# Kernel tuning notes

Measured on AMD Instinct MI355X. Metric: run time of the kernel, lower is better.

The kernel has to match this reference:

```python
import jax, jax.numpy as jnp
import numpy as np

S, T, C, L_GNN, L_TF, H = 8, 16, 128, 3, 2, 4
B = 512
FF = 4 * C
EPS = 1e-5


def setup_inputs() -> dict:
    key = jax.random.key(0)
    ks = jax.random.split(key, 24)
    w = lambda k, shape: jax.random.normal(k, shape, jnp.float32) * 0.05
    inp = {}
    inp["xx"] = jax.random.randint(ks[0], (B, T, S, S, S), 0, 3, dtype=jnp.int32)
    inp["ss"] = jax.random.uniform(ks[1], (B, 1), jnp.float32)
    # DynamicGNNv2 params
    inp["Win"] = w(ks[2], (C, 5)); inp["b_in"] = w(ks[3], (C,))
    inp["Wl"] = w(ks[4], (L_GNN, C, C)); inp["bl"] = w(ks[5], (L_GNN, C))   # SAGEConv lin_l (neighbors)
    inp["Wr"] = w(ks[6], (L_GNN, C, C))                                      # SAGEConv lin_r (root, no bias)
    inp["ln_g"] = jnp.ones((C,), jnp.float32); inp["ln_b"] = jnp.zeros((C,), jnp.float32)  # shared LayerNorm
    # TransformerEncoder params (norm_first, relu, dropout=0 at eval)
    inp["Wqkv"] = w(ks[7], (L_TF, 3 * C, C)); inp["bqkv"] = w(ks[8], (L_TF, 3 * C))
    inp["Wo"] = w(ks[9], (L_TF, C, C)); inp["bo"] = w(ks[10], (L_TF, C))
    inp["ln1_g"] = jnp.ones((L_TF, C), jnp.float32); inp["ln1_b"] = jnp.zeros((L_TF, C), jnp.float32)
    inp["ln2_g"] = jnp.ones((L_TF, C), jnp.float32); inp["ln2_b"] = jnp.zeros((L_TF, C), jnp.float32)
    inp["W1"] = w(ks[11], (L_TF, FF, C)); inp["b1"] = w(ks[12], (L_TF, FF))
    inp["W2"] = w(ks[13], (L_TF, C, FF)); inp["b2"] = w(ks[14], (L_TF, C))
    inp["Wact"] = w(ks[15], (C, S ** 3)); inp["bact"] = w(ks[16], (C,))
    inp["Wsc"] = w(ks[17], (C, 1)); inp["bsc"] = w(ks[18], (C,))
    return inp


def layernorm(x, g, b):
    mu = x.mean(-1, keepdims=True)
    var = ((x - mu) ** 2).mean(-1, keepdims=True)
    return (x - mu) * jax.lax.rsqrt(var + EPS) * g + b


def reference(xx, ss, Win, b_in, Wl, bl, Wr, ln_g, ln_b, Wqkv, bqkv, Wo, bo,
              ln1_g, ln1_b, ln2_g, ln2_b, W1, b1, W2, b2, Wact, bact, Wsc, bsc):
    Bc = xx.shape[0]
    S3 = S ** 3
    frame0 = xx[:, 0].reshape(Bc, S3).astype(jnp.float32)            # (B,S^3)
    m = (frame0 != 0).astype(jnp.float32)                            # active-node mask
    grid = jnp.arange(S3)
    i, j, k = grid // (S * S), (grid // S) % S, grid % S
    coord = jnp.stack([i, j, k], -1).astype(jnp.float32) / (S - 1)   # (S^3,3)
    feat = jnp.concatenate([
        jnp.broadcast_to(coord, (Bc, S3, 3)),
        (frame0 / 2.0)[..., None],
        jnp.broadcast_to((ss / S)[:, None, :], (Bc, S3, 1)),
    ], -1)                                                            # (B,S^3,5)
    x = feat @ Win.T + b_in                                           # lin_in
    mm = m[..., None]
    n = m.sum(-1, keepdims=True)[..., None]                           # nodes per graph (B,1,1)
    for l in range(L_GNN):
        # complete graph (no self loops): mean over neighbors = (sum_active - self)/(N-1)
        s = (x * mm).sum(1, keepdims=True)                            # (B,1,C)
        neigh = jnp.where(n > 1, (s - x) / jnp.maximum(n - 1.0, 1.0), 0.0)
        h = neigh @ Wl[l].T + bl[l] + x @ Wr[l].T                     # SAGEConv
        x = layernorm(jax.nn.relu(h), ln_g, ln_b)
    full = x * mm                                                     # scatter-fill into dense (B,S^3,C)
    # pooling matmul: mean over each i/j/k slice -> (B,3S,C)
    poolW = jnp.concatenate([
        (i[None, :] == jnp.arange(S)[:, None]).astype(jnp.float32),
        (j[None, :] == jnp.arange(S)[:, None]).astype(jnp.float32),
        (k[None, :] == jnp.arange(S)[:, None]).astype(jnp.float32),
    ], 0)                                                             # (3S,S^3)
    gnn_emb = jnp.einsum('ps,bsc->bpc', poolW, full) / poolW.sum(1)[None, :, None]
    # transformer over past actions
    a = xx[:, 1:].reshape(Bc, T - 1, S3).astype(jnp.float32) @ Wact.T + bact
    Hd = C // H
    scale = 1.0 / np.sqrt(Hd).astype(np.float32)
    split_heads = lambda t: t.reshape(Bc, -1, H, Hd).transpose(0, 2, 1, 3)
    for l in range(L_TF):
        h1 = layernorm(a, ln1_g[l], ln1_b[l])
        q, kk, v = jnp.split(h1 @ Wqkv[l].T + bqkv[l], 3, axis=-1)
        q, kk, v = split_heads(q), split_heads(kk), split_heads(v)
        att = jax.nn.softmax(jnp.einsum('bhqd,bhkd->bhqk', q, kk) * scale, -1)
        o = jnp.einsum('bhqk,bhkd->bhqd', att, v).transpose(0, 2, 1, 3).reshape(Bc, -1, C)
        a = a + (o @ Wo[l].T + bo[l])
        h2 = layernorm(a, ln2_g[l], ln2_b[l])
        a = a + (jax.nn.relu(h2 @ W1[l].T + b1[l]) @ W2[l].T + b2[l])
    act_emb = a.mean(1)                                               # (B,C)
    mv_emb = jax.nn.relu(ss @ Wsc.T + bsc)                            # (B,C)
    return jnp.concatenate([gnn_emb, act_emb[:, None], mv_emb[:, None]], 1)  # (B,3S+2,C)
```

## Files before the change

### kernel.cpp

```cpp
#include <hip/hip_runtime.h>
#include <hip/hip_bf16.h>
#include <string.h>

typedef __hip_bfloat16 bf16;
typedef __attribute__((ext_vector_type(8))) short short8;
typedef __attribute__((ext_vector_type(4))) float f32x4;

#define Bsz 512
#define S3  512
#define Tsz 16
#define Cc  128
#define TT  15
#define EPSv 1e-5f

__device__ __forceinline__ float u2f(unsigned short u) {
    return __uint_as_float(((unsigned)u) << 16);
}
__device__ __forceinline__ float ulo(unsigned u) { return __uint_as_float(u << 16); }
__device__ __forceinline__ float uhi(unsigned u) { return __uint_as_float(u & 0xffff0000u); }
__device__ __forceinline__ unsigned short f2bu(float v) {
    bf16 h = __float2bfloat16(v);
    unsigned short u; memcpy(&u, &h, 2); return u;
}
__device__ __forceinline__ unsigned short bfr16(float a) {
    unsigned u = __float_as_uint(a);
    u = u + 0x7fffu + ((u >> 16) & 1u);
    return (unsigned short)(u >> 16);
}
__device__ __forceinline__ unsigned fpack2(float a, float b) {
    unsigned r;
    asm("v_cvt_pk_bf16_f32 %0, %1, %2" : "=v"(r) : "v"(a), "v"(b));
    return r;
}
__device__ __forceinline__ float dot4(float4 a, float4 b) {
    return a.x*b.x + a.y*b.y + a.z*b.z + a.w*b.w;
}


__global__ __launch_bounds__(256) void k_tpack(const float* __restrict__ src,
                                               float* __restrict__ dst,
                                               int NR, int NK)
{
    __shared__ float tile[32][33];
    int k0 = blockIdx.x * 32, r0 = blockIdx.y * 32;
    int lr = threadIdx.x >> 5, lk = threadIdx.x & 31;
    for (int i = lr; i < 32; i += 8)
        tile[i][lk] = src[(size_t)(r0 + i) * NK + k0 + lk];
    __syncthreads();
    int c = threadIdx.x & 31, k4 = threadIdx.x >> 5;
    float4 v;
    v.x = tile[c][k4 * 4 + 0]; v.y = tile[c][k4 * 4 + 1];
    v.z = tile[c][k4 * 4 + 2]; v.w = tile[c][k4 * 4 + 3];
    ((float4*)dst)[(size_t)(k0 / 4 + k4) * NR + r0 + c] = v;
}

__global__ __launch_bounds__(256) void k_cvt5(
    const float* __restrict__ s0, const float* __restrict__ s1,
    const float* __restrict__ s2, const float* __restrict__ s3,
    const float* __restrict__ s4, ushort* __restrict__ dst)
{
    int i = blockIdx.x * 256 + threadIdx.x;
    if (i >= 114688) return;
    const float* src; int rel;
    if (i < 16384)      { src = s0; rel = i; }
    else if (i < 40960) { src = s1; rel = i - 16384; }
    else if (i < 49152) { src = s2; rel = i - 40960; }
    else if (i < 81920) { src = s3; rel = i - 49152; }
    else                { src = s4; rel = i - 81920; }
    float4 v = ((const float4*)src)[rel];
    ushort4 o;
    o.x = f2bu(v.x); o.y = f2bu(v.y); o.z = f2bu(v.z); o.w = f2bu(v.w);
    ((ushort4*)dst)[i] = o;
}

__global__ __launch_bounds__(256) void k_wpack(
    const float* __restrict__ Wl, const float* __restrict__ Wr,
    ushort* __restrict__ WB)
{
    int l = blockIdx.x, w = blockIdx.y;
    const float* src = (w == 0 ? Wl : Wr) + l * 16384;
    ushort* dst = WB + (size_t)(l * 2 + w) * 32 * 512;
    for (int item = threadIdx.x; item < 2048; item += 256) {
        int f = item >> 6, lane = item & 63;
        int t = f >> 2, ks = f & 3, ml = lane & 15, q = lane >> 4;
        int n = t * 16 + ml;
        const float* sA = src + n * 128 + 32 * ks + q * 4;
        const float* sB = sA + 16;
        float4 a = *(const float4*)sA;
        float4 b = *(const float4*)sB;
        ushort4 o0, o1;
        o0.x = f2bu(a.x); o0.y = f2bu(b.x); o0.z = f2bu(a.y); o0.w = f2bu(b.y);
        o1.x = f2bu(a.z); o1.y = f2bu(b.z); o1.z = f2bu(a.w); o1.w = f2bu(b.w);
        ushort* dp = dst + (size_t)f * 512 + lane * 8;
        *(ushort4*)dp = o0;
        *(ushort4*)(dp + 4) = o1;
    }
}

__global__ __launch_bounds__(512, 2) void k_torso(
    const int* __restrict__ xx, const float* __restrict__ ss,
    const float* __restrict__ Win, const float* __restrict__ b_in,
    const ushort* __restrict__ WB,
    const float4* __restrict__ WlP, const float* __restrict__ blv,
    const float* __restrict__ lng, const float* __restrict__ lnb,
    float* __restrict__ out)
{
    __shared__ ushort X[512 * 136];
    __shared__ float  mC[512];
    __shared__ float  sred[8 * 128];
    __shared__ float  ssc[128];
    __shared__ float  sbase[128];
    __shared__ float  gln[128], bln[128];
    __shared__ float  scnt[8];
    __shared__ float  invS;

    int b = blockIdx.x, tid = threadIdx.x;
    int wv = tid >> 6, lane = tid & 63;
    int ml = lane & 15, quad = lane >> 4;

    {
        int cp = lane;
        int co0 = 32 * (cp >> 4) + (cp & 15), co1 = co0 + 16;
        const int* x0 = xx + (size_t)b * Tsz * S3;
        float f4c = ss[b] * (1.0f / 8.0f);
        float a0 = Win[co0*5+0], a1 = Win[co0*5+1], a2 = Win[co0*5+2], a3 = Win[co0*5+3];
        float c0 = Win[co1*5+0], c1 = Win[co1*5+1], c2 = Win[co1*5+2], c3 = Win[co1*5+3];
        float ba = b_in[co0] + f4c * Win[co0*5+4];
        float bc = b_in[co1] + f4c * Win[co1*5+4];
        float sp0 = 0.f, sp1 = 0.f; int cnt = 0;
        for (int node = wv; node < S3; node += 8) {
            int f0 = x0[node];
            float m = (f0 != 0) ? 1.f : 0.f;
            float ci = (float)(node >> 6) * (1.f / 7.f);
            float cj = (float)((node >> 3) & 7) * (1.f / 7.f);
            float ck = (float)(node & 7) * (1.f / 7.f);
            float ft = (float)f0 * 0.5f;
            float v0 = ba + ci * a0 + cj * a1 + ck * a2 + ft * a3;
            float v1 = bc + ci * c0 + cj * c1 + ck * c2 + ft * c3;
            ((unsigned*)(X + node * 136))[cp] = fpack2(v0, v1);
            sp0 += v0 * m; sp1 += v1 * m;
            cnt += (f0 != 0);
            if (cp == 0) mC[node] = m;
        }
        sred[wv * 128 + co0] = sp0;
        sred[wv * 128 + co1] = sp1;
        if (cp == 0) scnt[wv] = (float)cnt;
    }
    if (tid < 128) { gln[tid] = lng[tid]; bln[tid] = lnb[tid]; }
    __syncthreads();
    if (tid == 0) {
        float n = 0.f;
#pragma unroll
        for (int g = 0; g < 8; g++) n += scnt[g];
        invS = (n > 1.f) ? 1.f / (n - 1.f) : 0.f;
    }
    __syncthreads();
    if (tid < 128) {
        float s = 0.f;
#pragma unroll
        for (int g = 0; g < 8; g++) s += sred[g * 128 + tid];
        ssc[tid] = s * invS;
    }
    __syncthreads();
    if (tid < 128) {
        float a = blv[tid];
        for (int k4 = 0; k4 < 32; k4++)
            a += dot4(*(const float4*)(ssc + k4 * 4), WlP[k4 * 384 + tid]);
        sbase[tid] = a;
    }
    __syncthreads();

    float ninv = -invS;

    for (int l = 0; l < 3; l++) {
        bool last = (l == 2);
        float sp[8];
#pragma unroll
        for (int t = 0; t < 8; t++) sp[t] = 0.f;

        f32x4 acc[8][4];
#pragma unroll
        for (int t = 0; t < 8; t++)
#pragma unroll
            for (int mm = 0; mm < 4; mm++) acc[t][mm] = (f32x4){0.f, 0.f, 0.f, 0.f};

        const ushort* xrb = X + (wv * 64 + ml) * 136 + quad * 8;

#pragma unroll 1
        for (int pass = 0; pass < 2; pass++) {
            const ushort* wp = WB + ((size_t)(l * 2 + pass) * 32) * 512 + lane * 8;
#pragma unroll
            for (int ks = 0; ks < 4; ks++) {
                short8 a[4];
#pragma unroll
                for (int mm = 0; mm < 4; mm++)
                    a[mm] = *(const short8*)(xrb + mm * 16 * 136 + ks * 32);
#pragma unroll
                for (int t = 0; t < 8; t++) {
                    short8 bg = *(const short8*)(wp + (size_t)(t * 4 + ks) * 512);
#pragma unroll
                    for (int mm = 0; mm < 4; mm++)
                        acc[t][mm] = __builtin_amdgcn_mfma_f32_16x16x32_bf16(a[mm], bg, acc[t][mm], 0, 0, 0);
                }
            }
            if (pass == 0) {
#pragma unroll
                for (int t = 0; t < 8; t++)
#pragma unroll
                    for (int mm = 0; mm < 4; mm++)
#pragma unroll
                        for (int r = 0; r < 4; r++)
                            acc[t][mm][r] *= ninv;
            }
        }

        float bse[8], gg[8], be[8];
#pragma unroll
        for (int t = 0; t < 8; t++) {
            bse[t] = sbase[t * 16 + ml];
            gg[t]  = gln[t * 16 + ml];
            be[t]  = bln[t * 16 + ml];
        }
#pragma unroll
        for (int mm = 0; mm < 4; mm++) {
#pragma unroll
            for (int r = 0; r < 4; r++) {
                int row = wv * 64 + mm * 16 + quad * 4 + r;
                float v[8];
                float s = 0.f, q = 0.f;
#pragma unroll
                for (int t = 0; t < 8; t++) {
                    float vv = fmaxf(acc[t][mm][r] + bse[t], 0.f);
                    v[t] = vv;
                    s += vv; q = fmaf(vv, vv, q);
                }
#pragma unroll
                for (int off = 1; off <= 8; off <<= 1) {
                    s += __shfl_xor(s, off, 64);
                    q += __shfl_xor(q, off, 64);
                }
                float mu = s * (1.f / 128.f);
                float rs = rsqrtf(q * (1.f / 128.f) - mu * mu + EPSv);
                float mrow = mC[row];
                unsigned* xr32 = (unsigned*)(X + row * 136);
                if (last) {
#pragma unroll
                    for (int t2 = 0; t2 < 4; t2++) {
                        float y0 = ((v[2*t2]   - mu) * rs * gg[2*t2]   + be[2*t2])   * mrow;
                        float y1 = ((v[2*t2+1] - mu) * rs * gg[2*t2+1] + be[2*t2+1]) * mrow;
                        xr32[t2 * 16 + ml] = fpack2(y0, y1);
                    }
                } else {
#pragma unroll
                    for (int t2 = 0; t2 < 4; t2++) {
                        float y0 = (v[2*t2]   - mu) * rs * gg[2*t2]   + be[2*t2];
                        float y1 = (v[2*t2+1] - mu) * rs * gg[2*t2+1] + be[2*t2+1];
                        sp[2*t2]   = fmaf(y0, mrow, sp[2*t2]);
                        sp[2*t2+1] = fmaf(y1, mrow, sp[2*t2+1]);
                        xr32[t2 * 16 + ml] = fpack2(y0, y1);
                    }
                }
            }
        }

        if (!last) {
#pragma unroll
            for (int t = 0; t < 8; t++) {
                sp[t] += __shfl_xor(sp[t], 16, 64);
                sp[t] += __shfl_xor(sp[t], 32, 64);
            }
            if (quad == 0) {
#pragma unroll
                for (int t = 0; t < 8; t++) sred[wv * 128 + t * 16 + ml] = sp[t];
            }
            __syncthreads();
            if (tid < 128) {
                float s = 0.f;
#pragma unroll
                for (int g = 0; g < 8; g++) s += sred[g * 128 + tid];
                ssc[tid] = s * invS;
            }
            __syncthreads();
            if (tid < 128) {
                float a = blv[(l + 1) * 128 + tid];
                for (int k4 = 0; k4 < 32; k4++)
                    a += dot4(*(const float4*)(ssc + k4 * 4), WlP[k4 * 384 + (l + 1) * 128 + tid]);
                sbase[tid] = a;
            }
            __syncthreads();
        }
    }
    __syncthreads();

    for (int item = tid; item < 768; item += 512) {
        int c4 = item & 31, p = item >> 5;
        int axis = p >> 3, idx = p & 7;
        float4 sum = {0.f, 0.f, 0.f, 0.f};
        for (int t = 0; t < 64; t++) {
            int node;
            if (axis == 0)      node = idx * 64 + t;
            else if (axis == 1) node = (t >> 3) * 64 + idx * 8 + (t & 7);
            else                node = t * 8 + idx;
            uint2 pk = *(const uint2*)(X + node * 136 + c4 * 4);
            sum.x += ulo(pk.x);
            sum.y += uhi(pk.x);
            sum.z += ulo(pk.y);
            sum.w += uhi(pk.y);
        }
        int E0 = 32 * (c4 >> 3) + 2 * (c4 & 7);
        float* ob = out + (size_t)b * 26 * Cc + p * Cc;
        float2 lo = {sum.x * (1.f / 64.f), sum.z * (1.f / 64.f)};
        float2 hi = {sum.y * (1.f / 64.f), sum.w * (1.f / 64.f)};
        *(float2*)(ob + E0)      = lo;
        *(float2*)(ob + E0 + 16) = hi;
    }
}

__global__ __launch_bounds__(256) void k_tf3(
    const int* __restrict__ xx, const float* __restrict__ ss,
    const ushort* __restrict__ WactB, const float* __restrict__ bact,
    const ushort* __restrict__ WqkvB, const float* __restrict__ bqkv,
    const ushort* __restrict__ WoB, const float* __restrict__ bo,
    const float* __restrict__ ln1g, const float* __restrict__ ln1b,
    const float* __restrict__ ln2g, const float* __restrict__ ln2b,
    const ushort* __restrict__ W1B, const float* __restrict__ b1v,
    const ushort* __restrict__ W2B, const float* __restrict__ b2v,
    const float* __restrict__ Wsc, const float* __restrict__ bsc,
    float* __restrict__ out)
{
    __shared__ float  As[TT * 132];
    __shared__ ushort Qs[16 * 392];
    __shared__ ushort Ab[16 * 136];
    __shared__ ushort Hs[16 * 136];
    __shared__ ushort Fs[16 * 520];
    __shared__ float  Att[60 * 16];
    __shared__ float  mu_s[TT], rs_s[TT];

    int b = blockIdx.x, tid = threadIdx.x;
    int wv = tid >> 6, lane = tid & 63;
    int ml = lane & 15, quad = lane >> 4;

    const int* xa = xx + (size_t)b * Tsz * S3 + S3;
    for (int f = tid; f < TT * 512; f += 256) {
        int t = f >> 9, s = f & 511;
        Fs[t * 520 + s] = bfr16((float)xa[t * 512 + s]);
    }
    __syncthreads();

    {
        f32x4 acc[2];
#pragma unroll
        for (int i = 0; i < 2; i++) acc[i] = (f32x4){0.f, 0.f, 0.f, 0.f};
        const ushort* ar = Fs + ml * 520 + quad * 8;
        for (int ks = 0; ks < 16; ks++) {
            short8 a = *(const short8*)(ar + ks * 32);
#pragma unroll
            for (int i = 0; i < 2; i++) {
                int n0 = (wv * 2 + i) * 16;
                short8 bfr = *(const short8*)(WactB + (size_t)(n0 + ml) * 512 + quad * 8 + ks * 32);
                acc[i] = __builtin_amdgcn_mfma_f32_16x16x32_bf16(a, bfr, acc[i], 0, 0, 0);
            }
        }
#pragma unroll
        for (int i = 0; i < 2; i++) {
            int col = (wv * 2 + i) * 16 + ml;
            float bb = bact[col];
#pragma unroll
            for (int r = 0; r < 4; r++) {
                int row = quad * 4 + r;
                if (row < TT) As[row * 132 + col] = acc[i][r] + bb;
            }
        }
    }
    __syncthreads();

    for (int l = 0; l < 2; l++) {
        const float* bq  = bqkv + l * 384;
        const float* bol = bo + l * 128;
        const float* g1  = ln1g + l * 128; const float* be1 = ln1b + l * 128;
        const float* g2  = ln2g + l * 128; const float* be2 = ln2b + l * 128;
        const float* b1l = b1v + l * 512;  const float* b2l = b2v + l * 128;

        for (int r = wv; r < TT; r += 4) {
            float2 v = *(const float2*)(As + r * 132 + lane * 2);
            float s = v.x + v.y, q = v.x * v.x + v.y * v.y;
            for (int off = 32; off; off >>= 1) {
                s += __shfl_xor(s, off, 64);
                q += __shfl_xor(q, off, 64);
            }
            if (lane == 0) {
                float mu = s * (1.f / 128.f);
                mu_s[r] = mu;
                rs_s[r] = rsqrtf(q * (1.f / 128.f) - mu * mu + EPSv);
            }
        }
        __syncthreads();
        for (int f = tid; f < TT * 64; f += 256) {
            int t = f >> 6, cp = f & 63;
            float mu = mu_s[t], rs = rs_s[t];
            float x0 = (As[t * 132 + 2 * cp]     - mu) * rs * g1[2 * cp]     + be1[2 * cp];
            float x1 = (As[t * 132 + 2 * cp + 1] - mu) * rs * g1[2 * cp + 1] + be1[2 * cp + 1];
            ((unsigned*)(Ab + t * 136))[cp] = fpack2(x0, x1);
        }
        __syncthreads();

        {
            short8 a[4];
            const ushort* ar = Ab + ml * 136 + quad * 8;
#pragma unroll
            for (int ks = 0; ks < 4; ks++) a[ks] = *(const short8*)(ar + ks * 32);
#pragma unroll
            for (int i = 0; i < 6; i++) {
                int n0 = (wv * 6 + i) * 16;
                f32x4 acc = (f32x4){0.f, 0.f, 0.f, 0.f};
                const ushort* wb = WqkvB + (size_t)(l * 384 + n0 + ml) * 128 + quad * 8;
#pragma unroll
                for (int ks = 0; ks < 4; ks++) {
                    short8 bfr = *(const short8*)(wb + ks * 32);
                    acc = __builtin_amdgcn_mfma_f32_16x16x32_bf16(a[ks], bfr, acc, 0, 0, 0);
                }
                int col = n0 + ml;
                float bb = bq[col];
#pragma unroll
                for (int r = 0; r < 4; r++) {
                    int row = quad * 4 + r;
                    if (row < TT) Qs[row * 392 + col] = bfr16(acc[r] + bb);
                }
            }
        }
        __syncthreads();

        if (tid < 60) {
            int h = tid / 15, tq = tid % 15;
            const ushort* qp = Qs + tq * 392 + h * 32;
            float sc[TT];
            float mx = -1e30f;
#pragma unroll
            for (int tk = 0; tk < TT; tk++) {
                const ushort* kp = Qs + tk * 392 + 128 + h * 32;
                float d = 0.f;
#pragma unroll
                for (int u = 0; u < 32; u += 4) {
                    uint2 qa = *(const uint2*)(qp + u);
                    uint2 ka = *(const uint2*)(kp + u);
                    d += ulo(qa.x) * ulo(ka.x) + uhi(qa.x) * uhi(ka.x)
                       + ulo(qa.y) * ulo(ka.y) + uhi(qa.y) * uhi(ka.y);
                }
                d *= 0.17677669529663689f;
                sc[tk] = d; mx = fmaxf(mx, d);
            }
            float sum = 0.f;
#pragma unroll
            for (int tk = 0; tk < TT; tk++) { float e = __expf(sc[tk] - mx); sc[tk] = e; sum += e; }
            float r = 1.f / sum;
#pragma unroll
            for (int tk = 0; tk < TT; tk++) Att[tid * 16 + tk] = sc[tk] * r;
        }
        __syncthreads();

        for (int f = tid; f < TT * 64; f += 256) {
            int t = f >> 6, cp = f & 63;
            int h = cp >> 4;
            const float* ap = Att + (h * 15 + t) * 16;
            const ushort* vp = Qs + 256 + 2 * cp;
            float a0 = 0.f, a1 = 0.f;
#pragma unroll
            for (int tk = 0; tk < TT; tk++) {
                float w = ap[tk];
                unsigned pk = *(const unsigned*)(vp + tk * 392);
                a0 += w * ulo(pk);
                a1 += w * uhi(pk);
            }
            ((unsigned*)(Hs + t * 136))[cp] = fpack2(a0, a1);
        }
        __syncthreads();

        {
            short8 a[4];
            const ushort* ar = Hs + ml * 136 + quad * 8;
#pragma unroll
            for (int ks = 0; ks < 4; ks++) a[ks] = *(const short8*)(ar + ks * 32);
#pragma unroll
            for (int i = 0; i < 2; i++) {
                int n0 = (wv * 2 + i) * 16;
                f32x4 acc = (f32x4){0.f, 0.f, 0.f, 0.f};
                const ushort* wb = WoB + (size_t)(l * 128 + n0 + ml) * 128 + quad * 8;
#pragma unroll
                for (int ks = 0; ks < 4; ks++) {
                    short8 bfr = *(const short8*)(wb + ks * 32);
                    acc = __builtin_amdgcn_mfma_f32_16x16x32_bf16(a[ks], bfr, acc, 0, 0, 0);
                }
                int col = n0 + ml;
                float bb = bol[col];
#pragma unroll
                for (int r = 0; r < 4; r++) {
                    int row = quad * 4 + r;
                    if (row < TT) As[row * 132 + col] += acc[r] + bb;
                }
            }
        }
        __syncthreads();

        for (int r = wv; r < TT; r += 4) {
            float2 v = *(const float2*)(As + r * 132 + lane * 2);
            float s = v.x + v.y, q = v.x * v.x + v.y * v.y;
            for (int off = 32; off; off >>= 1) {
                s += __shfl_xor(s, off, 64);
                q += __shfl_xor(q, off, 64);
            }
            if (lane == 0) {
                float mu = s * (1.f / 128.f);
                mu_s[r] = mu;
                rs_s[r] = rsqrtf(q * (1.f / 128.f) - mu * mu + EPSv);
            }
        }
        __syncthreads();
        for (int f = tid; f < TT * 64; f += 256) {
            int t = f >> 6, cp = f & 63;
            float mu = mu_s[t], rs = rs_s[t];
            float x0 = (As[t * 132 + 2 * cp]     - mu) * rs * g2[2 * cp]     + be2[2 * cp];
            float x1 = (As[t * 132 + 2 * cp + 1] - mu) * rs * g2[2 * cp + 1] + be2[2 * cp + 1];
            ((unsigned*)(Ab + t * 136))[cp] = fpack2(x0, x1);
        }
        __syncthreads();

        {
            short8 a[4];
            const ushort* ar = Ab + ml * 136 + quad * 8;
#pragma unroll
            for (int ks = 0; ks < 4; ks++) a[ks] = *(const short8*)(ar + ks * 32);
#pragma unroll
            for (int i = 0; i < 8; i++) {
                int n0 = (wv * 8 + i) * 16;
                f32x4 acc = (f32x4){0.f, 0.f, 0.f, 0.f};
                const ushort* wb = W1B + (size_t)(l * 512 + n0 + ml) * 128 + quad * 8;
#pragma unroll
                for (int ks = 0; ks < 4; ks++) {
                    short8 bfr = *(const short8*)(wb + ks * 32);
                    acc = __builtin_amdgcn_mfma_f32_16x16x32_bf16(a[ks], bfr, acc, 0, 0, 0);
                }
                int col = n0 + ml;
                float bb = b1l[col];
#pragma unroll
                for (int r = 0; r < 4; r++) {
                    int row = quad * 4 + r;
                    if (row < TT) Fs[row * 520 + col] = bfr16(fmaxf(acc[r] + bb, 0.f));
                }
            }
        }
        __syncthreads();

        {
            f32x4 acc[2];
#pragma unroll
            for (int i = 0; i < 2; i++) acc[i] = (f32x4){0.f, 0.f, 0.f, 0.f};
            const ushort* ar = Fs + ml * 520 + quad * 8;
            for (int ks = 0; ks < 16; ks++) {
                short8 a = *(const short8*)(ar + ks * 32);
#pragma unroll
                for (int i = 0; i < 2; i++) {
                    int n0 = (wv * 2 + i) * 16;
                    short8 bfr = *(const short8*)(W2B + (size_t)(l * 128 + n0 + ml) * 512 + quad * 8 + ks * 32);
                    acc[i] = __builtin_amdgcn_mfma_f32_16x16x32_bf16(a, bfr, acc[i], 0, 0, 0);
                }
            }
#pragma unroll
            for (int i = 0; i < 2; i++) {
                int col = (wv * 2 + i) * 16 + ml;
                float bb = b2l[col];
#pragma unroll
                for (int r = 0; r < 4; r++) {
                    int row = quad * 4 + r;
                    if (row < TT) As[row * 132 + col] += acc[i][r] + bb;
                }
            }
        }
        __syncthreads();
    }

    if (tid < 128) {
        float s = 0.f;
#pragma unroll
        for (int t = 0; t < TT; t++) s += As[t * 132 + tid];
        out[(size_t)b * 26 * Cc + 24 * Cc + tid] = s * (1.f / 15.f);
    } else if (tid < 256) {
        int co = tid - 128;
        float v = ss[b] * Wsc[co] + bsc[co];
        out[(size_t)b * 26 * Cc + 25 * Cc + co] = fmaxf(v, 0.f);
    }
}

extern "C" void kernel_launch(void* const* d_in, const int* in_sizes, int n_in,
                              void* d_out, int out_size, void* d_ws, size_t ws_size,
                              hipStream_t stream)
{
    (void)in_sizes; (void)n_in; (void)out_size; (void)ws_size;
    const int*   xx   = (const int*)d_in[0];
    const float* ss   = (const float*)d_in[1];
    const float* Win  = (const float*)d_in[2];
    const float* b_in = (const float*)d_in[3];
    const float* Wl   = (const float*)d_in[4];
    const float* bl   = (const float*)d_in[5];
    const float* Wr   = (const float*)d_in[6];
    const float* lng  = (const float*)d_in[7];
    const float* lnb  = (const float*)d_in[8];
    const float* Wqkv = (const float*)d_in[9];
    const float* bqkv = (const float*)d_in[10];
    const float* Wo   = (const float*)d_in[11];
    const float* bo   = (const float*)d_in[12];
    const float* ln1g = (const float*)d_in[13];
    const float* ln1b = (const float*)d_in[14];
    const float* ln2g = (const float*)d_in[15];
    const float* ln2b = (const float*)d_in[16];
    const float* W1   = (const float*)d_in[17];
    const float* b1   = (const float*)d_in[18];
    const float* W2   = (const float*)d_in[19];
    const float* b2   = (const float*)d_in[20];
    const float* Wact = (const float*)d_in[21];
    const float* bact = (const float*)d_in[22];
    const float* Wsc  = (const float*)d_in[23];
    const float* bsc  = (const float*)d_in[24];
    float* out = (float*)d_out;

    char* ws = (char*)d_ws;
    size_t off = 0;
    float* WlT  = (float*)(ws + off); off += 384 * 128 * 4;
    ushort* WB    = (ushort*)(ws + off); off += (size_t)3 * 2 * 128 * 128 * 2;
    ushort* WactB = (ushort*)(ws + off); off += 128 * 512 * 2;
    ushort* WqkvB = (ushort*)(ws + off); off += 768 * 128 * 2;
    ushort* WoB   = (ushort*)(ws + off); off += 256 * 128 * 2;
    ushort* W1B   = (ushort*)(ws + off); off += 1024 * 128 * 2;
    ushort* W2B   = (ushort*)(ws + off); off += 256 * 512 * 2;

    k_tpack<<<dim3(4, 12), 256, 0, stream>>>(Wl, WlT, 384, 128);
    k_cvt5<<<448, 256, 0, stream>>>(Wact, Wqkv, Wo, W1, W2, WactB);
    k_wpack<<<dim3(3, 2), 256, 0, stream>>>(Wl, Wr, WB);

    k_torso<<<Bsz, 512, 0, stream>>>(xx, ss, Win, b_in, WB,
                                     (const float4*)WlT, bl, lng, lnb, out);

    k_tf3<<<Bsz, 256, 0, stream>>>(xx, ss,
                                   WactB, bact, WqkvB, bqkv, WoB, bo,
                                   ln1g, ln1b, ln2g, ln2b,
                                   W1B, b1, W2B, b2,
                                   Wsc, bsc, out);
}
```

Measured before the change: 338.0 us.

## Fold SAGE neighbor and root weights into one combined matrix staged in LDS

Each GNN layer previously ran two MFMA passes over the same node features: one against Wl, scaled by -1/(n-1), and one against Wr. The new code builds a combined bf16 weight (-invS*Wl + Wr) per half of the output channels, stages it in LDS, and runs a single MFMA pass, halving GNN matrix work. It also spreads the 128-wide bias matvec over all 512 threads, and counts active nodes with a ballot from an LDS-cached frame. In exchange there is extra LDS use (16KB) and an extra bf16 rounding of the combined weights, with more barriers per layer.

```diff
diff --git a/kernel.cpp b/kernel.cpp
--- a/kernel.cpp
+++ b/kernel.cpp
@@ -11,6 +11,7 @@
 #define Tsz 16
 #define Cc  128
 #define TT  15
+#define XP  136
 #define EPSv 1e-5f
 
 __device__ __forceinline__ float u2f(unsigned short u) {
@@ -105,8 +106,9 @@
     const float* __restrict__ lng, const float* __restrict__ lnb,
     float* __restrict__ out)
 {
-    __shared__ ushort X[512 * 136];
-    __shared__ float  mC[512];
+    __shared__ ushort X[512 * XP];
+    __shared__ ushort Ds[16 * 512];
+    __shared__ ushort mCu[512];
     __shared__ float  sred[8 * 128];
     __shared__ float  ssc[128];
     __shared__ float  sbase[128];
@@ -118,18 +120,30 @@
     int wv = tid >> 6, lane = tid & 63;
     int ml = lane & 15, quad = lane >> 4;
 
+    int* fC = (int*)Ds;
+
+    const int* x0 = xx + (size_t)b * Tsz * S3;
+    {
+        int f0 = x0[tid];
+        fC[tid] = f0;
+        mCu[tid] = (f0 != 0) ? (ushort)0x3F80 : (ushort)0;
+        unsigned long long bal = __ballot(f0 != 0);
+        if (lane == 0) scnt[wv] = (float)__popcll(bal);
+    }
+    if (tid < 128) { gln[tid] = lng[tid]; bln[tid] = lnb[tid]; }
+    __syncthreads();
+
     {
         int cp = lane;
         int co0 = 32 * (cp >> 4) + (cp & 15), co1 = co0 + 16;
-        const int* x0 = xx + (size_t)b * Tsz * S3;
         float f4c = ss[b] * (1.0f / 8.0f);
         float a0 = Win[co0*5+0], a1 = Win[co0*5+1], a2 = Win[co0*5+2], a3 = Win[co0*5+3];
         float c0 = Win[co1*5+0], c1 = Win[co1*5+1], c2 = Win[co1*5+2], c3 = Win[co1*5+3];
         float ba = b_in[co0] + f4c * Win[co0*5+4];
         float bc = b_in[co1] + f4c * Win[co1*5+4];
-        float sp0 = 0.f, sp1 = 0.f; int cnt = 0;
+        float sp0 = 0.f, sp1 = 0.f;
         for (int node = wv; node < S3; node += 8) {
-            int f0 = x0[node];
+            int f0 = fC[node];
             float m = (f0 != 0) ? 1.f : 0.f;
             float ci = (float)(node >> 6) * (1.f / 7.f);
             float cj = (float)((node >> 3) & 7) * (1.f / 7.f);
@@ -137,16 +151,12 @@
             float ft = (float)f0 * 0.5f;
             float v0 = ba + ci * a0 + cj * a1 + ck * a2 + ft * a3;
             float v1 = bc + ci * c0 + cj * c1 + ck * c2 + ft * c3;
-            ((unsigned*)(X + node * 136))[cp] = fpack2(v0, v1);
+            ((unsigned*)(X + node * XP))[cp] = fpack2(v0, v1);
             sp0 += v0 * m; sp1 += v1 * m;
-            cnt += (f0 != 0);
-            if (cp == 0) mC[node] = m;
         }
         sred[wv * 128 + co0] = sp0;
         sred[wv * 128 + co1] = sp1;
-        if (cp == 0) scnt[wv] = (float)cnt;
-    }
-    if (tid < 128) { gln[tid] = lng[tid]; bln[tid] = lnb[tid]; }
+    }
     __syncthreads();
     if (tid == 0) {
         float n = 0.f;
@@ -162,12 +172,17 @@
         ssc[tid] = s * invS;
     }
     __syncthreads();
-    if (tid < 128) {
-        float a = blv[tid];
-        for (int k4 = 0; k4 < 32; k4++)
-            a += dot4(*(const float4*)(ssc + k4 * 4), WlP[k4 * 384 + tid]);
-        sbase[tid] = a;
-    }
+    {
+        int part = tid >> 7, c = tid & 127;
+        float a = 0.f;
+#pragma unroll
+        for (int k4 = part * 8; k4 < part * 8 + 8; k4++)
+            a += dot4(*(const float4*)(ssc + k4 * 4), WlP[k4 * 384 + c]);
+        sred[part * 128 + c] = a;
+    }
+    __syncthreads();
+    if (tid < 128)
+        sbase[tid] = blv[tid] + sred[tid] + sred[128 + tid] + sred[256 + tid] + sred[384 + tid];
     __syncthreads();
 
     float ninv = -invS;
@@ -184,34 +199,38 @@
 #pragma unroll
             for (int mm = 0; mm < 4; mm++) acc[t][mm] = (f32x4){0.f, 0.f, 0.f, 0.f};
 
-        const ushort* xrb = X + (wv * 64 + ml) * 136 + quad * 8;
+        const ushort* xrb = X + (wv * 64 + ml) * XP + quad * 8;
 
 #pragma unroll 1
-        for (int pass = 0; pass < 2; pass++) {
-            const ushort* wp = WB + ((size_t)(l * 2 + pass) * 32) * 512 + lane * 8;
+        for (int h = 0; h < 2; h++) {
+            const ushort* wl = WB + ((size_t)(l * 2 + 0) * 32 + h * 16) * 512;
+            const ushort* wr = WB + ((size_t)(l * 2 + 1) * 32 + h * 16) * 512;
+            for (int g = tid; g < 1024; g += 512) {
+                uint4 ul = *(const uint4*)(wl + g * 8);
+                uint4 ur = *(const uint4*)(wr + g * 8);
+                uint4 d;
+                d.x = fpack2(fmaf(ninv, ulo(ul.x), ulo(ur.x)), fmaf(ninv, uhi(ul.x), uhi(ur.x)));
+                d.y = fpack2(fmaf(ninv, ulo(ul.y), ulo(ur.y)), fmaf(ninv, uhi(ul.y), uhi(ur.y)));
+                d.z = fpack2(fmaf(ninv, ulo(ul.z), ulo(ur.z)), fmaf(ninv, uhi(ul.z), uhi(ur.z)));
+                d.w = fpack2(fmaf(ninv, ulo(ul.w), ulo(ur.w)), fmaf(ninv, uhi(ul.w), uhi(ur.w)));
+                *(uint4*)(Ds + g * 8) = d;
+            }
+            __syncthreads();
 #pragma unroll
             for (int ks = 0; ks < 4; ks++) {
                 short8 a[4];
 #pragma unroll
                 for (int mm = 0; mm < 4; mm++)
-                    a[mm] = *(const short8*)(xrb + mm * 16 * 136 + ks * 32);
-#pragma unroll
-                for (int t = 0; t < 8; t++) {
-                    short8 bg = *(const short8*)(wp + (size_t)(t * 4 + ks) * 512);
+                    a[mm] = *(const short8*)(xrb + mm * 16 * XP + ks * 32);
+#pragma unroll
+                for (int tq = 0; tq < 4; tq++) {
+                    short8 bg = *(const short8*)(Ds + (size_t)(tq * 4 + ks) * 512 + lane * 8);
 #pragma unroll
                     for (int mm = 0; mm < 4; mm++)
-                        acc[t][mm] = __builtin_amdgcn_mfma_f32_16x16x32_bf16(a[mm], bg, acc[t][mm], 0, 0, 0);
-                }
-            }
-            if (pass == 0) {
-#pragma unroll
-                for (int t = 0; t < 8; t++)
-#pragma unroll
-                    for (int mm = 0; mm < 4; mm++)
-#pragma unroll
-                        for (int r = 0; r < 4; r++)
-                            acc[t][mm][r] *= ninv;
-            }
+                        acc[h * 4 + tq][mm] = __builtin_amdgcn_mfma_f32_16x16x32_bf16(a[mm], bg, acc[h * 4 + tq][mm], 0, 0, 0);
+                }
+            }
+            __syncthreads();
         }
 
         float bse[8], gg[8], be[8];
@@ -241,8 +260,8 @@
                 }
                 float mu = s * (1.f / 128.f);
                 float rs = rsqrtf(q * (1.f / 128.f) - mu * mu + EPSv);
-                float mrow = mC[row];
-                unsigned* xr32 = (unsigned*)(X + row * 136);
+                float mrow = u2f(mCu[row]);
+                unsigned* xr32 = (unsigned*)(X + row * XP);
                 if (last) {
 #pragma unroll
                     for (int t2 = 0; t2 < 4; t2++) {
@@ -281,12 +300,17 @@
                 ssc[tid] = s * invS;
             }
             __syncthreads();
-            if (tid < 128) {
-                float a = blv[(l + 1) * 128 + tid];
-                for (int k4 = 0; k4 < 32; k4++)
-                    a += dot4(*(const float4*)(ssc + k4 * 4), WlP[k4 * 384 + (l + 1) * 128 + tid]);
-                sbase[tid] = a;
-            }
+            {
+                int part = tid >> 7, c = tid & 127;
+                float a = 0.f;
+#pragma unroll
+                for (int k4 = part * 8; k4 < part * 8 + 8; k4++)
+                    a += dot4(*(const float4*)(ssc + k4 * 4), WlP[k4 * 384 + (l + 1) * 128 + c]);
+                sred[part * 128 + c] = a;
+            }
+            __syncthreads();
+            if (tid < 128)
+                sbase[tid] = blv[(l + 1) * 128 + tid] + sred[tid] + sred[128 + tid] + sred[256 + tid] + sred[384 + tid];
             __syncthreads();
         }
     }
@@ -301,7 +325,7 @@
             if (axis == 0)      node = idx * 64 + t;
             else if (axis == 1) node = (t >> 3) * 64 + idx * 8 + (t & 7);
             else                node = t * 8 + idx;
-            uint2 pk = *(const uint2*)(X + node * 136 + c4 * 4);
+            uint2 pk = *(const uint2*)(X + node * XP + c4 * 4);
             sum.x += ulo(pk.x);
             sum.y += uhi(pk.x);
             sum.z += ulo(pk.y);
```

New measurement: 481.9 us. 1.43x slower.
